# Optimization experiments

Measured on AMD Instinct MI355X. Metric: run time of the kernel, lower is better.

Reference implementation:

```python
import jax, jax.numpy as jnp
import numpy as np

NEG_SLOPE = 0.2
EPS = 1e-16

N_NODES = 50000
N_EDGES = 800000
IN_C = 256
HID_C = 64
HEADS = 4
OUT_C = 128
N_GRAPHS = 100


def setup_inputs() -> dict:
    key = jax.random.key(0)
    ks = jax.random.split(key, 12)
    x = jax.random.normal(ks[0], (N_NODES, IN_C), dtype=jnp.float32)
    edge_index = jax.random.randint(ks[1], (2, N_EDGES), 0, N_NODES, dtype=jnp.int64)
    batch = jnp.sort(jax.random.randint(ks[2], (N_NODES,), 0, N_GRAPHS, dtype=jnp.int64))
    s1 = 1.0 / np.sqrt(IN_C)
    s2 = 1.0 / np.sqrt(HEADS * HID_C)
    W1 = jax.random.uniform(ks[3], (IN_C, HEADS * HID_C), jnp.float32, -s1, s1)
    att_src1 = jax.random.uniform(ks[4], (HEADS, HID_C), jnp.float32, -s1, s1)
    att_dst1 = jax.random.uniform(ks[5], (HEADS, HID_C), jnp.float32, -s1, s1)
    bias1 = jnp.zeros((HEADS * HID_C,), jnp.float32)
    W2 = jax.random.uniform(ks[6], (HEADS * HID_C, OUT_C), jnp.float32, -s2, s2)
    att_src2 = jax.random.uniform(ks[7], (1, OUT_C), jnp.float32, -s2, s2)
    att_dst2 = jax.random.uniform(ks[8], (1, OUT_C), jnp.float32, -s2, s2)
    bias2 = jnp.zeros((OUT_C,), jnp.float32)
    return {"x": x, "W1": W1, "att_src1": att_src1, "att_dst1": att_dst1,
            "bias1": bias1, "W2": W2, "att_src2": att_src2, "att_dst2": att_dst2,
            "bias2": bias2, "edge_index": edge_index, "batch": batch,
            "num_graphs": N_GRAPHS}


def gat_conv(x, W, att_src, att_dst, bias, src, dst, heads, ch):
    # x: [N, F_in]; W: [F_in, heads*ch]; att_*: [heads, ch]
    n = x.shape[0]
    h = (x @ W).reshape(n, heads, ch)                      # [N, H, C]
    a_src = jnp.sum(h * att_src[None], axis=-1)            # [N, H]
    a_dst = jnp.sum(h * att_dst[None], axis=-1)            # [N, H]
    alpha = a_src[src] + a_dst[dst]                        # [E, H]
    alpha = jax.nn.leaky_relu(alpha, NEG_SLOPE)
    # segment softmax over destination nodes (every node has a self-loop)
    amax = jax.ops.segment_max(alpha, dst, num_segments=n)
    e = jnp.exp(alpha - amax[dst])
    denom = jax.ops.segment_sum(e, dst, num_segments=n)
    alpha = e / (denom[dst] + EPS)                         # [E, H]
    msg = h[src] * alpha[:, :, None]                       # [E, H, C]
    out = jax.ops.segment_sum(msg, dst, num_segments=n)    # [N, H, C]
    return out.reshape(n, heads * ch) + bias


def reference(x, W1, att_src1, att_dst1, bias1, W2, att_src2, att_dst2, bias2,
              edge_index, batch, num_graphs):
    n = x.shape[0]
    loops = jnp.arange(n, dtype=edge_index.dtype)
    src = jnp.concatenate([edge_index[0], loops])
    dst = jnp.concatenate([edge_index[1], loops])
    h = gat_conv(x, W1, att_src1, att_dst1, bias1, src, dst, HEADS, HID_C)
    h = jax.nn.relu(h)
    h = gat_conv(h, W2, att_src2, att_dst2, bias2, src, dst, 1, OUT_C)
    h = jax.nn.relu(h)
    # global mean pool over graphs
    sums = jax.ops.segment_sum(h, batch, num_segments=num_graphs)
    cnt = jax.ops.segment_sum(jnp.ones((n, 1), h.dtype), batch, num_segments=num_graphs)
    return sums / jnp.maximum(cnt, 1.0)
```

## Files before the change

kernel.cpp:

```cpp
#include <hip/hip_runtime.h>
#include <hip/hip_bf16.h>
#include <hip/hip_fp16.h>

#define N_NODES 50000
#define N_EDGES 800000
#define E_TOT   (N_EDGES + N_NODES)
#define IN_C    256
#define H1C     256
#define HEADS   4
#define HID_C   64
#define OUT_C   128
#define N_GRAPHS 100
#define NEG_SLOPE 0.2f
#define EPS_F 1e-16f

#define NBUCKET 391
#define SORT_BLOCKS 104
#define EDGES_PER_SB 8192
#define BH_STRIDE 392
#define STAGE_CAP 3072

#define PREP_BHIST_BLOCKS  104
#define PREP_CAST_BLOCKS   12500
#define PREP_W1_BLOCKS     256
#define PREP_W2_BLOCKS     128
#define PREP_BOUNDS_BLOCKS 196
#define PREP_DOUT_BLOCKS   50
#define PREP_TOTAL (PREP_BHIST_BLOCKS + PREP_CAST_BLOCKS + PREP_W1_BLOCKS + PREP_W2_BLOCKS + PREP_BOUNDS_BLOCKS + PREP_DOUT_BLOCKS)

typedef _Float16 half8_t __attribute__((ext_vector_type(8)));
typedef float f32x4 __attribute__((ext_vector_type(4)));

__global__ __launch_bounds__(256) void prep_kernel(const float* __restrict__ x,
                                                   _Float16* __restrict__ xh,
                                                   const float* __restrict__ W1,
                                                   _Float16* __restrict__ W1t,
                                                   const float* __restrict__ W2,
                                                   _Float16* __restrict__ W2t,
                                                   const int* __restrict__ ei,
                                                   int* __restrict__ bhist,
                                                   const int* __restrict__ batch,
                                                   int* __restrict__ gstart,
                                                   float* __restrict__ d_out) {
    __shared__ int bh[NBUCKET];
    int b = blockIdx.x;
    int tid = threadIdx.x;
    if (b < PREP_BHIST_BLOCKS) {
        for (int t = tid; t < NBUCKET; t += 256) bh[t] = 0;
        __syncthreads();
        int base = b * EDGES_PER_SB;
#pragma unroll 4
        for (int k = 0; k < EDGES_PER_SB / 256; ++k) {
            int idx = base + k * 256 + tid;
            int d = -1;
            if (idx < N_EDGES) d = ei[N_EDGES + idx];
            else if (idx < E_TOT) d = idx - N_EDGES;
            if (d >= 0 && d < N_NODES) atomicAdd(&bh[d >> 7], 1);
        }
        __syncthreads();
        for (int t = tid; t < NBUCKET; t += 256)
            bhist[b * BH_STRIDE + t] = bh[t];
        return;
    }
    b -= PREP_BHIST_BLOCKS;
    if (b < PREP_CAST_BLOCKS) {
        int idx = b * 256 + tid;
        float4 v = reinterpret_cast<const float4*>(x)[idx];
        union { _Float16 h[4]; uint2 u; } p;
        p.h[0] = (_Float16)v.x; p.h[1] = (_Float16)v.y;
        p.h[2] = (_Float16)v.z; p.h[3] = (_Float16)v.w;
        reinterpret_cast<uint2*>(xh)[idx] = p.u;
        return;
    }
    b -= PREP_CAST_BLOCKS;
    if (b < PREP_W1_BLOCKS) {
        int idx = b * 256 + tid;
        int n = idx >> 8, k = idx & 255;
        W1t[idx] = (_Float16)W1[k * 256 + n];
        return;
    }
    b -= PREP_W1_BLOCKS;
    if (b < PREP_W2_BLOCKS) {
        int idx = b * 256 + tid;
        int n = idx >> 8, k = idx & 255;
        W2t[idx] = (_Float16)W2[k * 128 + n];
        return;
    }
    b -= PREP_W2_BLOCKS;
    if (b < PREP_BOUNDS_BLOCKS) {
        int idx = b * 256 + tid;
        if (idx >= N_NODES) return;
        int g = batch[idx];
        if (g < 0) g = 0; if (g >= N_GRAPHS) g = N_GRAPHS - 1;
        if (idx == 0) {
            for (int j = 0; j <= g; ++j) gstart[j] = 0;
        } else {
            int gp = batch[idx - 1];
            if (gp < 0) gp = 0; if (gp >= N_GRAPHS) gp = N_GRAPHS - 1;
            for (int j = gp + 1; j <= g; ++j) gstart[j] = idx;
        }
        if (idx == N_NODES - 1) {
            for (int j = g + 1; j <= N_GRAPHS; ++j) gstart[j] = N_NODES;
        }
        return;
    }
    b -= PREP_BOUNDS_BLOCKS;
    {
        int idx = b * 256 + tid;
        if (idx < N_GRAPHS * 128) d_out[idx] = 0.f;
    }
}

__global__ __launch_bounds__(64) void bucket_scan(int* __restrict__ bhist,
                                                  int* __restrict__ btot) {
    int j = blockIdx.x;
    int lane = threadIdx.x;
    int carry = 0;
    for (int b0 = 0; b0 < SORT_BLOCKS; b0 += 64) {
        int b = b0 + lane;
        int v = (b < SORT_BLOCKS) ? bhist[b * BH_STRIDE + j] : 0;
        int inc = v;
#pragma unroll
        for (int off = 1; off < 64; off <<= 1) {
            int u = __shfl_up(inc, off);
            if (lane >= off) inc += u;
        }
        if (b < SORT_BLOCKS) bhist[b * BH_STRIDE + j] = inc - v + carry;
        carry += __shfl(inc, 63);
    }
    if (lane == 0) btot[j] = carry;
}

__global__ __launch_bounds__(512) void bucket_base(const int* __restrict__ btot,
                                                   int* __restrict__ bbase) {
    __shared__ int lds[512];
    int t = threadIdx.x;
    int v = (t < NBUCKET) ? btot[t] : 0;
    lds[t] = v;
    __syncthreads();
#pragma unroll
    for (int off = 1; off < 512; off <<= 1) {
        int u = (t >= off) ? lds[t - off] : 0;
        __syncthreads();
        lds[t] += u;
        __syncthreads();
    }
    if (t < NBUCKET) bbase[t] = lds[t] - v;
    if (t == NBUCKET - 1) bbase[NBUCKET] = lds[t];
}

__global__ __launch_bounds__(256) void bucket_bin(const int* __restrict__ ei,
                                                  const int* __restrict__ bbase,
                                                  const int* __restrict__ bhist,
                                                  int* __restrict__ ebuf) {
    __shared__ int cur[NBUCKET];
    int tid = threadIdx.x;
    for (int t = tid; t < NBUCKET; t += 256)
        cur[t] = bbase[t] + bhist[blockIdx.x * BH_STRIDE + t];
    __syncthreads();
    int base = blockIdx.x * EDGES_PER_SB;
#pragma unroll 4
    for (int k = 0; k < EDGES_PER_SB / 256; ++k) {
        int idx = base + k * 256 + tid;
        int s = 0, d = -1;
        if (idx < N_EDGES) { s = ei[idx]; d = ei[N_EDGES + idx]; }
        else if (idx < E_TOT) { s = idx - N_EDGES; d = s; }
        if (d >= 0 && d < N_NODES) {
            int p = atomicAdd(&cur[d >> 7], 1);
            ebuf[p] = (s & 0xFFFF) | ((d & 127) << 16);
        }
    }
}

__global__ __launch_bounds__(256) void bucket_sort(const int* __restrict__ bbase,
                                                   const int* __restrict__ ebuf,
                                                   int* __restrict__ ssrc,
                                                   int* __restrict__ row_ptr) {
    __shared__ int cnt[128];
    __shared__ int sc[128];
    __shared__ int stage[STAGE_CAP];
    int j = blockIdx.x;
    int tid = threadIdx.x;
    int jn0 = j << 7;
    int nNodes = N_NODES - jn0; if (nNodes > 128) nNodes = 128;
    int lo = bbase[j];
    int hi = bbase[j + 1];
    int span = hi - lo;
    if (tid < 128) cnt[tid] = 0;
    __syncthreads();
    for (int t = lo + tid; t < hi; t += 256)
        atomicAdd(&cnt[(ebuf[t] >> 16) & 127], 1);
    __syncthreads();
    if (tid < 128) sc[tid] = cnt[tid];
    __syncthreads();
#pragma unroll
    for (int off = 1; off < 128; off <<= 1) {
        int u = (tid >= off && tid < 128) ? sc[tid - off] : 0;
        __syncthreads();
        if (tid < 128) sc[tid] += u;
        __syncthreads();
    }
    if (tid < 128) {
        int excl = sc[tid] - cnt[tid];
        if (tid < nNodes) row_ptr[jn0 + tid] = lo + excl;
        cnt[tid] = excl;
    }
    if (j == NBUCKET - 1 && tid == 0) row_ptr[N_NODES] = hi;
    __syncthreads();
    if (span <= STAGE_CAP) {
        for (int t = lo + tid; t < hi; t += 256) {
            int v = ebuf[t];
            int p = atomicAdd(&cnt[(v >> 16) & 127], 1);
            stage[p] = v & 0xFFFF;
        }
        __syncthreads();
        for (int t = tid; t < span; t += 256) ssrc[lo + t] = stage[t];
    } else {
        for (int t = lo + tid; t < hi; t += 256) {
            int v = ebuf[t];
            int p = atomicAdd(&cnt[(v >> 16) & 127], 1);
            if (p >= 0 && p < span) ssrc[lo + p] = v & 0xFFFF;
        }
    }
}

__global__ __launch_bounds__(256) void gemm_mfma_kernel(const _Float16* __restrict__ A,
                                                        const _Float16* __restrict__ Bt,
                                                        _Float16* __restrict__ C,
                                                        int mode,
                                                        const float* __restrict__ attS,
                                                        const float* __restrict__ attD,
                                                        float* __restrict__ a_src_o,
                                                        float* __restrict__ a_dst_o,
                                                        int M, int N) {
    __shared__ _Float16 As[128][56];
    __shared__ _Float16 Bs[128][56];
    __shared__ float lds_ps[128];
    __shared__ float lds_pd[128];
    const int tid = threadIdx.x;
    const int tileM = blockIdx.x * 128;
    const int tileN = blockIdx.y * 128;
    const int w = tid >> 6, lane = tid & 63;
    const int wm = (w >> 1) * 64, wn = (w & 1) * 64;
    const int quad = lane >> 4, mlane = lane & 15;
    const int srow = tid >> 2;
    const int schunk = (tid & 3) * 8;

    f32x4 zero = {0.f, 0.f, 0.f, 0.f};
    f32x4 acc[4][4];
#pragma unroll
    for (int i = 0; i < 4; ++i)
#pragma unroll
        for (int j = 0; j < 4; ++j) acc[i][j] = zero;

    const uint4* Av = reinterpret_cast<const uint4*>(A);
    const uint4* Bv = reinterpret_cast<const uint4*>(Bt);
    const int r0 = tileM + srow, r1 = r0 + 64;
    const bool ok0 = r0 < M, ok1 = r1 < M;
    const int bn0 = tileN + srow, bn1 = bn0 + 64;
    const uint4 z4 = make_uint4(0, 0, 0, 0);

    for (int k0 = 0; k0 < 256; k0 += 32) {
        const int kc = (k0 >> 3) + (tid & 3);
        uint4 a0 = ok0 ? Av[(size_t)r0 * 32 + kc] : z4;
        uint4 a1 = ok1 ? Av[(size_t)r1 * 32 + kc] : z4;
        uint4 b0 = Bv[(size_t)bn0 * 32 + kc];
        uint4 b1 = Bv[(size_t)bn1 * 32 + kc];
        __syncthreads();
        *reinterpret_cast<uint4*>(&As[srow][schunk]) = a0;
        *reinterpret_cast<uint4*>(&As[srow + 64][schunk]) = a1;
        *reinterpret_cast<uint4*>(&Bs[srow][schunk]) = b0;
        *reinterpret_cast<uint4*>(&Bs[srow + 64][schunk]) = b1;
        __syncthreads();
        half8_t af[4], bf[4];
#pragma unroll
        for (int mt = 0; mt < 4; ++mt)
            af[mt] = *reinterpret_cast<const half8_t*>(&As[wm + mt * 16 + mlane][quad * 8]);
#pragma unroll
        for (int nt = 0; nt < 4; ++nt)
            bf[nt] = *reinterpret_cast<const half8_t*>(&Bs[wn + nt * 16 + mlane][quad * 8]);
#pragma unroll
        for (int mt = 0; mt < 4; ++mt)
#pragma unroll
            for (int nt = 0; nt < 4; ++nt)
                acc[mt][nt] = __builtin_amdgcn_mfma_f32_16x16x32_f16(af[mt], bf[nt], acc[mt][nt], 0, 0, 0);
    }
#pragma unroll
    for (int mt = 0; mt < 4; ++mt) {
#pragma unroll
        for (int i = 0; i < 4; ++i) {
            int row = tileM + wm + mt * 16 + quad * 4 + i;
            if (row < M) {
                _Float16* cp = C + (size_t)row * N + tileN + wn;
#pragma unroll
                for (int nt = 0; nt < 4; ++nt)
                    cp[nt * 16 + mlane] = (_Float16)acc[mt][nt][i];
            }
        }
    }
    if (mode == 1) {
        int hd = (tileN + wn) >> 6;
        float as[4], ad[4];
#pragma unroll
        for (int nt = 0; nt < 4; ++nt) {
            as[nt] = attS[hd * 64 + nt * 16 + mlane];
            ad[nt] = attD[hd * 64 + nt * 16 + mlane];
        }
#pragma unroll
        for (int mt = 0; mt < 4; ++mt) {
#pragma unroll
            for (int i = 0; i < 4; ++i) {
                float ps = acc[mt][0][i] * as[0] + acc[mt][1][i] * as[1]
                         + acc[mt][2][i] * as[2] + acc[mt][3][i] * as[3];
                float pd = acc[mt][0][i] * ad[0] + acc[mt][1][i] * ad[1]
                         + acc[mt][2][i] * ad[2] + acc[mt][3][i] * ad[3];
#pragma unroll
                for (int off = 1; off < 16; off <<= 1) {
                    ps += __shfl_xor(ps, off);
                    pd += __shfl_xor(pd, off);
                }
                if (mlane == 0) {
                    int row = tileM + wm + mt * 16 + quad * 4 + i;
                    if (row < M) {
                        a_src_o[row * 4 + hd] = ps;
                        a_dst_o[row * 4 + hd] = pd;
                    }
                }
            }
        }
    } else if (mode == 2) {
        float as[4], ad[4];
#pragma unroll
        for (int nt = 0; nt < 4; ++nt) {
            as[nt] = attS[wn + nt * 16 + mlane];
            ad[nt] = attD[wn + nt * 16 + mlane];
        }
        float psa[4][4], pda[4][4];
#pragma unroll
        for (int mt = 0; mt < 4; ++mt) {
#pragma unroll
            for (int i = 0; i < 4; ++i) {
                float ps = acc[mt][0][i] * as[0] + acc[mt][1][i] * as[1]
                         + acc[mt][2][i] * as[2] + acc[mt][3][i] * as[3];
                float pd = acc[mt][0][i] * ad[0] + acc[mt][1][i] * ad[1]
                         + acc[mt][2][i] * ad[2] + acc[mt][3][i] * ad[3];
#pragma unroll
                for (int off = 1; off < 16; off <<= 1) {
                    ps += __shfl_xor(ps, off);
                    pd += __shfl_xor(pd, off);
                }
                psa[mt][i] = ps; pda[mt][i] = pd;
            }
        }
        __syncthreads();
        if (wn == 0 && mlane == 0) {
#pragma unroll
            for (int mt = 0; mt < 4; ++mt)
#pragma unroll
                for (int i = 0; i < 4; ++i) {
                    int lr = wm + mt * 16 + quad * 4 + i;
                    lds_ps[lr] = psa[mt][i];
                    lds_pd[lr] = pda[mt][i];
                }
        }
        __syncthreads();
        if (wn == 64 && mlane == 0) {
#pragma unroll
            for (int mt = 0; mt < 4; ++mt)
#pragma unroll
                for (int i = 0; i < 4; ++i) {
                    int lr = wm + mt * 16 + quad * 4 + i;
                    int row = tileM + lr;
                    if (row < M) {
                        a_src_o[row] = psa[mt][i] + lds_ps[lr];
                        a_dst_o[row] = pda[mt][i] + lds_pd[lr];
                    }
                }
        }
    }
}

__device__ __forceinline__ float lrelu(float x) { return x > 0.f ? x : NEG_SLOPE * x; }

__global__ __launch_bounds__(256) void edge1_kernel(const int* __restrict__ row_ptr,
                                                    const int* __restrict__ ssrc,
                                                    const __half* __restrict__ h1h,
                                                    const float* __restrict__ a_src,
                                                    const float* __restrict__ a_dst,
                                                    const float* __restrict__ bias,
                                                    __half* __restrict__ out) {
    int node = blockIdx.x * 4 + (threadIdx.x >> 6);
    int lane = threadIdx.x & 63;
    int hf   = lane >> 5;
    int cl   = lane & 31;
    int hd   = cl >> 3;
    int start = row_ptr[node], end = row_ptr[node + 1];
    int em1 = end - 1;
    float adh = a_dst[node * 4 + hd];

    const uint4* h1v = reinterpret_cast<const uint4*>(h1h);
    float4 aA0 = make_float4(0.f,0.f,0.f,0.f), aA1 = make_float4(0.f,0.f,0.f,0.f);
    float4 aB0 = make_float4(0.f,0.f,0.f,0.f), aB1 = make_float4(0.f,0.f,0.f,0.f);
    float s = 0.f;
    for (int e = start; e < end; e += 4) {
        int e0 = e + hf;
        int e1 = e + 2 + hf;
        int i0 = ssrc[e0 <= em1 ? e0 : em1];
        int i1 = ssrc[e1 <= em1 ? e1 : em1];
        float r0 = a_src[i0 * 4 + hd];
        float r1 = a_src[i1 * 4 + hd];
        uint4 q0 = h1v[(size_t)i0 * 32 + cl];
        uint4 q1 = h1v[(size_t)i1 * 32 + cl];
        float w0 = (e0 < end) ? __expf(lrelu(r0 + adh)) : 0.f;
        float w1 = (e1 < end) ? __expf(lrelu(r1 + adh)) : 0.f;
        s += w0 + w1;
        float2 f;
        f = __half22float2(*reinterpret_cast<const __half2*>(&q0.x)); aA0.x += w0*f.x; aA0.y += w0*f.y;
        f = __half22float2(*reinterpret_cast<const __half2*>(&q0.y)); aA0.z += w0*f.x; aA0.w += w0*f.y;
        f = __half22float2(*reinterpret_cast<const __half2*>(&q0.z)); aA1.x += w0*f.x; aA1.y += w0*f.y;
        f = __half22float2(*reinterpret_cast<const __half2*>(&q0.w)); aA1.z += w0*f.x; aA1.w += w0*f.y;
        f = __half22float2(*reinterpret_cast<const __half2*>(&q1.x)); aB0.x += w1*f.x; aB0.y += w1*f.y;
        f = __half22float2(*reinterpret_cast<const __half2*>(&q1.y)); aB0.z += w1*f.x; aB0.w += w1*f.y;
        f = __half22float2(*reinterpret_cast<const __half2*>(&q1.z)); aB1.x += w1*f.x; aB1.y += w1*f.y;
        f = __half22float2(*reinterpret_cast<const __half2*>(&q1.w)); aB1.z += w1*f.x; aB1.w += w1*f.y;
    }
    float4 c0, c1;
    c0.x = aA0.x + aB0.x; c0.y = aA0.y + aB0.y; c0.z = aA0.z + aB0.z; c0.w = aA0.w + aB0.w;
    c1.x = aA1.x + aB1.x; c1.y = aA1.y + aB1.y; c1.z = aA1.z + aB1.z; c1.w = aA1.w + aB1.w;
    c0.x += __shfl_xor(c0.x, 32); c0.y += __shfl_xor(c0.y, 32);
    c0.z += __shfl_xor(c0.z, 32); c0.w += __shfl_xor(c0.w, 32);
    c1.x += __shfl_xor(c1.x, 32); c1.y += __shfl_xor(c1.y, 32);
    c1.z += __shfl_xor(c1.z, 32); c1.w += __shfl_xor(c1.w, 32);
    s += __shfl_xor(s, 32);
    float inv = 1.0f / (s + EPS_F);
    if (lane < 32) {
        const float4* b4 = reinterpret_cast<const float4*>(bias);
        float4 b0 = b4[cl * 2], b1 = b4[cl * 2 + 1];
        union { _Float16 h[8]; uint4 u; } st;
        st.h[0] = (_Float16)fmaxf(c0.x * inv + b0.x, 0.f);
        st.h[1] = (_Float16)fmaxf(c0.y * inv + b0.y, 0.f);
        st.h[2] = (_Float16)fmaxf(c0.z * inv + b0.z, 0.f);
        st.h[3] = (_Float16)fmaxf(c0.w * inv + b0.w, 0.f);
        st.h[4] = (_Float16)fmaxf(c1.x * inv + b1.x, 0.f);
        st.h[5] = (_Float16)fmaxf(c1.y * inv + b1.y, 0.f);
        st.h[6] = (_Float16)fmaxf(c1.z * inv + b1.z, 0.f);
        st.h[7] = (_Float16)fmaxf(c1.w * inv + b1.w, 0.f);
        reinterpret_cast<uint4*>(out)[(size_t)node * 32 + cl] = st.u;
    }
}

__global__ __launch_bounds__(256) void edge2_kernel(const int* __restrict__ row_ptr,
                                                    const int* __restrict__ ssrc,
                                                    const __half* __restrict__ h2h,
                                                    const float* __restrict__ a_src,
                                                    const float* __restrict__ a_dst,
                                                    const float* __restrict__ bias,
                                                    float* __restrict__ out) {
    int lane = threadIdx.x & 63;
    int node = blockIdx.x * 8 + ((threadIdx.x >> 6) << 1) + (lane >> 5);
    int sub  = (lane >> 4) & 1;
    int cl   = lane & 15;
    int start = row_ptr[node], end = row_ptr[node + 1];
    int em1 = end - 1;
    float ad = a_dst[node];

    const uint4* h2v = reinterpret_cast<const uint4*>(h2h);
    float4 aA0 = make_float4(0.f,0.f,0.f,0.f), aA1 = make_float4(0.f,0.f,0.f,0.f);
    float4 aB0 = make_float4(0.f,0.f,0.f,0.f), aB1 = make_float4(0.f,0.f,0.f,0.f);
    float s = 0.f;
    for (int e = start; e < end; e += 4) {
        int e0 = e + sub;
        int e1 = e + 2 + sub;
        int i0 = ssrc[e0 <= em1 ? e0 : em1];
        int i1 = ssrc[e1 <= em1 ? e1 : em1];
        float r0 = a_src[i0];
        float r1 = a_src[i1];
        uint4 q0 = h2v[(size_t)i0 * 16 + cl];
        uint4 q1 = h2v[(size_t)i1 * 16 + cl];
        float w0 = (e0 < end) ? __expf(lrelu(r0 + ad)) : 0.f;
        float w1 = (e1 < end) ? __expf(lrelu(r1 + ad)) : 0.f;
        s += w0 + w1;
        float2 f;
        f = __half22float2(*reinterpret_cast<const __half2*>(&q0.x)); aA0.x += w0*f.x; aA0.y += w0*f.y;
        f = __half22float2(*reinterpret_cast<const __half2*>(&q0.y)); aA0.z += w0*f.x; aA0.w += w0*f.y;
        f = __half22float2(*reinterpret_cast<const __half2*>(&q0.z)); aA1.x += w0*f.x; aA1.y += w0*f.y;
        f = __half22float2(*reinterpret_cast<const __half2*>(&q0.w)); aA1.z += w0*f.x; aA1.w += w0*f.y;
        f = __half22float2(*reinterpret_cast<const __half2*>(&q1.x)); aB0.x += w1*f.x; aB0.y += w1*f.y;
        f = __half22float2(*reinterpret_cast<const __half2*>(&q1.y)); aB0.z += w1*f.x; aB0.w += w1*f.y;
        f = __half22float2(*reinterpret_cast<const __half2*>(&q1.z)); aB1.x += w1*f.x; aB1.y += w1*f.y;
        f = __half22float2(*reinterpret_cast<const __half2*>(&q1.w)); aB1.z += w1*f.x; aB1.w += w1*f.y;
    }
    float4 c0, c1;
    c0.x = aA0.x + aB0.x; c0.y = aA0.y + aB0.y; c0.z = aA0.z + aB0.z; c0.w = aA0.w + aB0.w;
    c1.x = aA1.x + aB1.x; c1.y = aA1.y + aB1.y; c1.z = aA1.z + aB1.z; c1.w = aA1.w + aB1.w;
    c0.x += __shfl_xor(c0.x, 16); c0.y += __shfl_xor(c0.y, 16);
    c0.z += __shfl_xor(c0.z, 16); c0.w += __shfl_xor(c0.w, 16);
    c1.x += __shfl_xor(c1.x, 16); c1.y += __shfl_xor(c1.y, 16);
    c1.z += __shfl_xor(c1.z, 16); c1.w += __shfl_xor(c1.w, 16);
    s += __shfl_xor(s, 16);
    float inv = 1.0f / (s + EPS_F);
    if (sub == 0) {
        const float4* b4 = reinterpret_cast<const float4*>(bias);
        float4 b0 = b4[cl * 2], b1 = b4[cl * 2 + 1];
        float4 o0, o1;
        o0.x = fmaxf(c0.x * inv + b0.x, 0.f);
        o0.y = fmaxf(c0.y * inv + b0.y, 0.f);
        o0.z = fmaxf(c0.z * inv + b0.z, 0.f);
        o0.w = fmaxf(c0.w * inv + b0.w, 0.f);
        o1.x = fmaxf(c1.x * inv + b1.x, 0.f);
        o1.y = fmaxf(c1.y * inv + b1.y, 0.f);
        o1.z = fmaxf(c1.z * inv + b1.z, 0.f);
        o1.w = fmaxf(c1.w * inv + b1.w, 0.f);
        float4* o4 = reinterpret_cast<float4*>(out) + (size_t)node * 32 + cl * 2;
        o4[0] = o0;
        o4[1] = o1;
    }
}

#define POOL_CHUNK 64
__global__ __launch_bounds__(128) void pool_kernel(const float* __restrict__ out2,
                                                   const int* __restrict__ batch,
                                                   const int* __restrict__ gstart,
                                                   float* __restrict__ d_out) {
    int c = threadIdx.x;
    int node0 = blockIdx.x * POOL_CHUNK;
    int nodeEnd = node0 + POOL_CHUNK; if (nodeEnd > N_NODES) nodeEnd = N_NODES;
    if (node0 >= N_NODES) return;
    int gprev = batch[node0];
    float acc = 0.f;
    for (int node = node0; node < nodeEnd; ++node) {
        int g = batch[node];
        if (g != gprev) {
            if (gprev >= 0 && gprev < N_GRAPHS) {
                float cnt = (float)(gstart[gprev + 1] - gstart[gprev]);
                if (cnt < 1.f) cnt = 1.f;
                atomicAdd(&d_out[gprev * 128 + c], acc / cnt);
            }
            acc = 0.f;
            gprev = g;
        }
        acc += out2[(size_t)node * 128 + c];
    }
    if (gprev >= 0 && gprev < N_GRAPHS) {
        float cnt = (float)(gstart[gprev + 1] - gstart[gprev]);
        if (cnt < 1.f) cnt = 1.f;
        atomicAdd(&d_out[gprev * 128 + c], acc / cnt);
    }
}

extern "C" void kernel_launch(void* const* d_in, const int* in_sizes, int n_in,
                              void* d_out_v, int out_size, void* d_ws, size_t ws_size,
                              hipStream_t stream) {
    const float* x      = (const float*)d_in[0];
    const float* W1     = (const float*)d_in[1];
    const float* att_s1 = (const float*)d_in[2];
    const float* att_d1 = (const float*)d_in[3];
    const float* bias1  = (const float*)d_in[4];
    const float* W2     = (const float*)d_in[5];
    const float* att_s2 = (const float*)d_in[6];
    const float* att_d2 = (const float*)d_in[7];
    const float* bias2  = (const float*)d_in[8];
    const int*   ei     = (const int*)d_in[9];
    const int*   batch  = (const int*)d_in[10];
    float* d_out = (float*)d_out_v;

    float* ws = (float*)d_ws;
    _Float16* xh    = (_Float16*)ws;
    _Float16* h1h   = (_Float16*)(ws + 6400000);
    _Float16* out1h = (_Float16*)(ws + 12800000);
    _Float16* h2h   = (_Float16*)ws;
    float*    out2  = ws + 6400000;
    float* a_src1 = ws + 19200000;
    float* a_dst1 = a_src1 + 200000;
    float* a_src2 = a_dst1 + 200000;
    float* a_dst2 = a_src2 + 50000;
    int* row_ptr  = (int*)(a_dst2 + 50000);
    int* ssrc     = row_ptr + 50016;
    int* ebuf     = ssrc + 850000;
    int* bhist    = ebuf + 851968;
    int* btot     = bhist + (SORT_BLOCKS * BH_STRIDE);
    int* bbase    = btot + 512;
    int* gstart   = bbase + 512;
    _Float16* W1t = (_Float16*)(gstart + 128);
    _Float16* W2t = W1t + 65536;

    prep_kernel<<<PREP_TOTAL, 256, 0, stream>>>(x, xh, W1, W1t, W2, W2t,
                                                ei, bhist, batch, gstart, d_out);

    bucket_scan<<<NBUCKET, 64, 0, stream>>>(bhist, btot);
    bucket_base<<<1, 512, 0, stream>>>(btot, bbase);
    bucket_bin<<<SORT_BLOCKS, 256, 0, stream>>>(ei, bbase, bhist, ebuf);
    bucket_sort<<<NBUCKET, 256, 0, stream>>>(bbase, ebuf, ssrc, row_ptr);

    {
        dim3 g((N_NODES + 127) / 128, H1C / 128);
        gemm_mfma_kernel<<<g, 256, 0, stream>>>(xh, W1t, h1h, 1,
                                                att_s1, att_d1, a_src1, a_dst1,
                                                N_NODES, H1C);
    }
    edge1_kernel<<<N_NODES / 4, 256, 0, stream>>>(row_ptr, ssrc, (const __half*)h1h,
                                                  a_src1, a_dst1, bias1, (__half*)out1h);

    {
        dim3 g((N_NODES + 127) / 128, OUT_C / 128);
        gemm_mfma_kernel<<<g, 256, 0, stream>>>(out1h, W2t, h2h, 2,
                                                att_s2, att_d2, a_src2, a_dst2,
                                                N_NODES, OUT_C);
    }
    edge2_kernel<<<N_NODES / 8, 256, 0, stream>>>(row_ptr, ssrc, (const __half*)h2h,
                                                  a_src2, a_dst2, bias2, out2);

    pool_kernel<<<(N_NODES + POOL_CHUNK - 1) / POOL_CHUNK, 128, 0, stream>>>(out2, batch, gstart, d_out);
}
```

Measured before the change: 302.2 us.

## Replace multi-pass bucket sort with atomic bucket offsets and fuse sort with GEMM1

Result: no change. 299.6 us (-0.9%).

```diff
diff --git a/kernel.cpp b/kernel.cpp
--- a/kernel.cpp
+++ b/kernel.cpp
@@ -15,18 +15,18 @@
 #define EPS_F 1e-16f
 
 #define NBUCKET 391
-#define SORT_BLOCKS 104
+#define BIN_BLOCKS 104
 #define EDGES_PER_SB 8192
-#define BH_STRIDE 392
-#define STAGE_CAP 3072
-
-#define PREP_BHIST_BLOCKS  104
+#define EBUF_CAP 4096
+#define STAGE_CAP 4096
+#define GEMM1_MB 391
+
 #define PREP_CAST_BLOCKS   12500
 #define PREP_W1_BLOCKS     256
 #define PREP_W2_BLOCKS     128
 #define PREP_BOUNDS_BLOCKS 196
-#define PREP_DOUT_BLOCKS   50
-#define PREP_TOTAL (PREP_BHIST_BLOCKS + PREP_CAST_BLOCKS + PREP_W1_BLOCKS + PREP_W2_BLOCKS + PREP_BOUNDS_BLOCKS + PREP_DOUT_BLOCKS)
+#define PREP_ZERO_BLOCKS   52
+#define PREP_TOTAL (PREP_CAST_BLOCKS + PREP_W1_BLOCKS + PREP_W2_BLOCKS + PREP_BOUNDS_BLOCKS + PREP_ZERO_BLOCKS)
 
 typedef _Float16 half8_t __attribute__((ext_vector_type(8)));
 typedef float f32x4 __attribute__((ext_vector_type(4)));
@@ -37,32 +37,12 @@
                                                    _Float16* __restrict__ W1t,
                                                    const float* __restrict__ W2,
                                                    _Float16* __restrict__ W2t,
-                                                   const int* __restrict__ ei,
-                                                   int* __restrict__ bhist,
                                                    const int* __restrict__ batch,
                                                    int* __restrict__ gstart,
+                                                   int* __restrict__ gcur,
                                                    float* __restrict__ d_out) {
-    __shared__ int bh[NBUCKET];
     int b = blockIdx.x;
     int tid = threadIdx.x;
-    if (b < PREP_BHIST_BLOCKS) {
-        for (int t = tid; t < NBUCKET; t += 256) bh[t] = 0;
-        __syncthreads();
-        int base = b * EDGES_PER_SB;
-#pragma unroll 4
-        for (int k = 0; k < EDGES_PER_SB / 256; ++k) {
-            int idx = base + k * 256 + tid;
-            int d = -1;
-            if (idx < N_EDGES) d = ei[N_EDGES + idx];
-            else if (idx < E_TOT) d = idx - N_EDGES;
-            if (d >= 0 && d < N_NODES) atomicAdd(&bh[d >> 7], 1);
-        }
-        __syncthreads();
-        for (int t = tid; t < NBUCKET; t += 256)
-            bhist[b * BH_STRIDE + t] = bh[t];
-        return;
-    }
-    b -= PREP_BHIST_BLOCKS;
     if (b < PREP_CAST_BLOCKS) {
         int idx = b * 256 + tid;
         float4 v = reinterpret_cast<const float4*>(x)[idx];
@@ -108,57 +88,37 @@
     {
         int idx = b * 256 + tid;
         if (idx < N_GRAPHS * 128) d_out[idx] = 0.f;
-    }
-}
-
-__global__ __launch_bounds__(64) void bucket_scan(int* __restrict__ bhist,
-                                                  int* __restrict__ btot) {
-    int j = blockIdx.x;
-    int lane = threadIdx.x;
-    int carry = 0;
-    for (int b0 = 0; b0 < SORT_BLOCKS; b0 += 64) {
-        int b = b0 + lane;
-        int v = (b < SORT_BLOCKS) ? bhist[b * BH_STRIDE + j] : 0;
-        int inc = v;
-#pragma unroll
-        for (int off = 1; off < 64; off <<= 1) {
-            int u = __shfl_up(inc, off);
-            if (lane >= off) inc += u;
-        }
-        if (b < SORT_BLOCKS) bhist[b * BH_STRIDE + j] = inc - v + carry;
-        carry += __shfl(inc, 63);
-    }
-    if (lane == 0) btot[j] = carry;
-}
-
-__global__ __launch_bounds__(512) void bucket_base(const int* __restrict__ btot,
-                                                   int* __restrict__ bbase) {
-    __shared__ int lds[512];
-    int t = threadIdx.x;
-    int v = (t < NBUCKET) ? btot[t] : 0;
-    lds[t] = v;
-    __syncthreads();
-#pragma unroll
-    for (int off = 1; off < 512; off <<= 1) {
-        int u = (t >= off) ? lds[t - off] : 0;
-        __syncthreads();
-        lds[t] += u;
-        __syncthreads();
-    }
-    if (t < NBUCKET) bbase[t] = lds[t] - v;
-    if (t == NBUCKET - 1) bbase[NBUCKET] = lds[t];
+        else {
+            int k = idx - N_GRAPHS * 128;
+            if (k < 512) gcur[k] = 0;
+        }
+    }
 }
 
 __global__ __launch_bounds__(256) void bucket_bin(const int* __restrict__ ei,
-                                                  const int* __restrict__ bbase,
-                                                  const int* __restrict__ bhist,
+                                                  int* __restrict__ gcur,
                                                   int* __restrict__ ebuf) {
-    __shared__ int cur[NBUCKET];
+    __shared__ int bh[NBUCKET];
+    __shared__ int bofs[NBUCKET];
     int tid = threadIdx.x;
-    for (int t = tid; t < NBUCKET; t += 256)
-        cur[t] = bbase[t] + bhist[blockIdx.x * BH_STRIDE + t];
+    for (int t = tid; t < NBUCKET; t += 256) bh[t] = 0;
     __syncthreads();
     int base = blockIdx.x * EDGES_PER_SB;
+#pragma unroll 4
+    for (int k = 0; k < EDGES_PER_SB / 256; ++k) {
+        int idx = base + k * 256 + tid;
+        int d = -1;
+        if (idx < N_EDGES) d = ei[N_EDGES + idx];
+        else if (idx < E_TOT) d = idx - N_EDGES;
+        if (d >= 0 && d < N_NODES) atomicAdd(&bh[d >> 7], 1);
+    }
+    __syncthreads();
+    for (int t = tid; t < NBUCKET; t += 256) {
+        int c = bh[t];
+        bofs[t] = (c > 0) ? atomicAdd(&gcur[t], c) : 0;
+        bh[t] = 0;
+    }
+    __syncthreads();
 #pragma unroll 4
     for (int k = 0; k < EDGES_PER_SB / 256; ++k) {
         int idx = base + k * 256 + tid;
@@ -166,60 +126,175 @@
         if (idx < N_EDGES) { s = ei[idx]; d = ei[N_EDGES + idx]; }
         else if (idx < E_TOT) { s = idx - N_EDGES; d = s; }
         if (d >= 0 && d < N_NODES) {
-            int p = atomicAdd(&cur[d >> 7], 1);
-            ebuf[p] = (s & 0xFFFF) | ((d & 127) << 16);
-        }
-    }
-}
-
-__global__ __launch_bounds__(256) void bucket_sort(const int* __restrict__ bbase,
-                                                   const int* __restrict__ ebuf,
-                                                   int* __restrict__ ssrc,
-                                                   int* __restrict__ row_ptr) {
-    __shared__ int cnt[128];
-    __shared__ int sc[128];
-    __shared__ int stage[STAGE_CAP];
-    int j = blockIdx.x;
-    int tid = threadIdx.x;
-    int jn0 = j << 7;
-    int nNodes = N_NODES - jn0; if (nNodes > 128) nNodes = 128;
-    int lo = bbase[j];
-    int hi = bbase[j + 1];
-    int span = hi - lo;
-    if (tid < 128) cnt[tid] = 0;
-    __syncthreads();
-    for (int t = lo + tid; t < hi; t += 256)
-        atomicAdd(&cnt[(ebuf[t] >> 16) & 127], 1);
-    __syncthreads();
-    if (tid < 128) sc[tid] = cnt[tid];
-    __syncthreads();
-#pragma unroll
-    for (int off = 1; off < 128; off <<= 1) {
-        int u = (tid >= off && tid < 128) ? sc[tid - off] : 0;
-        __syncthreads();
-        if (tid < 128) sc[tid] += u;
-        __syncthreads();
-    }
-    if (tid < 128) {
-        int excl = sc[tid] - cnt[tid];
-        if (tid < nNodes) row_ptr[jn0 + tid] = lo + excl;
-        cnt[tid] = excl;
-    }
-    if (j == NBUCKET - 1 && tid == 0) row_ptr[N_NODES] = hi;
-    __syncthreads();
-    if (span <= STAGE_CAP) {
-        for (int t = lo + tid; t < hi; t += 256) {
-            int v = ebuf[t];
+            int t = d >> 7;
+            int p = bofs[t] + atomicAdd(&bh[t], 1);
+            if (p < EBUF_CAP)
+                ebuf[t * EBUF_CAP + p] = (s & 0xFFFF) | ((d & 127) << 16);
+        }
+    }
+}
+
+__global__ __launch_bounds__(256) void sort_gemm1_kernel(const int* __restrict__ gcur,
+                                                         const int* __restrict__ ebuf,
+                                                         int* __restrict__ ssrc,
+                                                         int* __restrict__ row_ptr,
+                                                         const _Float16* __restrict__ A,
+                                                         const _Float16* __restrict__ Bt,
+                                                         _Float16* __restrict__ C,
+                                                         const float* __restrict__ attS,
+                                                         const float* __restrict__ attD,
+                                                         float* __restrict__ a_src_o,
+                                                         float* __restrict__ a_dst_o) {
+    __shared__ __align__(16) char smem[29696];
+    __shared__ int s_off;
+    const int tid = threadIdx.x;
+
+    if (blockIdx.x < NBUCKET) {
+        int* cnt   = reinterpret_cast<int*>(smem);
+        int* sc    = cnt + 128;
+        int* stage = sc + 128;
+        int j = blockIdx.x;
+        if (tid < 64) {
+            int acc = 0;
+            for (int i = tid; i < j; i += 64) {
+                int c = gcur[i];
+                acc += (c < EBUF_CAP) ? c : EBUF_CAP;
+            }
+#pragma unroll
+            for (int off = 32; off > 0; off >>= 1) acc += __shfl_down(acc, off);
+            if (tid == 0) s_off = acc;
+        }
+        if (tid < 128) cnt[tid] = 0;
+        __syncthreads();
+        int span = gcur[j]; if (span > EBUF_CAP) span = EBUF_CAP;
+        int lo = s_off;
+        const int* eb = ebuf + j * EBUF_CAP;
+        for (int t = tid; t < span; t += 256)
+            atomicAdd(&cnt[(eb[t] >> 16) & 127], 1);
+        __syncthreads();
+        if (tid < 128) sc[tid] = cnt[tid];
+        __syncthreads();
+#pragma unroll
+        for (int off = 1; off < 128; off <<= 1) {
+            int u = (tid >= off && tid < 128) ? sc[tid - off] : 0;
+            __syncthreads();
+            if (tid < 128) sc[tid] += u;
+            __syncthreads();
+        }
+        int jn0 = j << 7;
+        int nNodes = N_NODES - jn0; if (nNodes > 128) nNodes = 128;
+        if (tid < 128) {
+            int excl = sc[tid] - cnt[tid];
+            if (tid < nNodes) row_ptr[jn0 + tid] = lo + excl;
+            cnt[tid] = excl;
+        }
+        if (j == NBUCKET - 1 && tid == 0) row_ptr[N_NODES] = lo + span;
+        __syncthreads();
+        for (int t = tid; t < span; t += 256) {
+            int v = eb[t];
             int p = atomicAdd(&cnt[(v >> 16) & 127], 1);
             stage[p] = v & 0xFFFF;
         }
         __syncthreads();
         for (int t = tid; t < span; t += 256) ssrc[lo + t] = stage[t];
-    } else {
-        for (int t = lo + tid; t < hi; t += 256) {
-            int v = ebuf[t];
-            int p = atomicAdd(&cnt[(v >> 16) & 127], 1);
-            if (p >= 0 && p < span) ssrc[lo + p] = v & 0xFFFF;
+        return;
+    }
+
+    _Float16 (*As)[56] = reinterpret_cast<_Float16(*)[56]>(smem);
+    _Float16 (*Bs)[56] = reinterpret_cast<_Float16(*)[56]>(smem + 14336);
+    float* lds_ps = reinterpret_cast<float*>(smem + 28672);
+    float* lds_pd = reinterpret_cast<float*>(smem + 29184);
+    (void)lds_ps; (void)lds_pd;
+    int b2 = blockIdx.x - NBUCKET;
+    const int tileM = (b2 >= GEMM1_MB ? b2 - GEMM1_MB : b2) * 128;
+    const int tileN = (b2 >= GEMM1_MB) ? 128 : 0;
+    const int w = tid >> 6, lane = tid & 63;
+    const int wm = (w >> 1) * 64, wn = (w & 1) * 64;
+    const int quad = lane >> 4, mlane = lane & 15;
+    const int srow = tid >> 2;
+    const int schunk = (tid & 3) * 8;
+
+    f32x4 zero = {0.f, 0.f, 0.f, 0.f};
+    f32x4 acc[4][4];
+#pragma unroll
+    for (int i = 0; i < 4; ++i)
+#pragma unroll
+        for (int j = 0; j < 4; ++j) acc[i][j] = zero;
+
+    const uint4* Av = reinterpret_cast<const uint4*>(A);
+    const uint4* Bv = reinterpret_cast<const uint4*>(Bt);
+    const int r0 = tileM + srow, r1 = r0 + 64;
+    const bool ok0 = r0 < N_NODES, ok1 = r1 < N_NODES;
+    const int bn0 = tileN + srow, bn1 = bn0 + 64;
+    const uint4 z4 = make_uint4(0, 0, 0, 0);
+
+    for (int k0 = 0; k0 < 256; k0 += 32) {
+        const int kc = (k0 >> 3) + (tid & 3);
+        uint4 a0 = ok0 ? Av[(size_t)r0 * 32 + kc] : z4;
+        uint4 a1 = ok1 ? Av[(size_t)r1 * 32 + kc] : z4;
+        uint4 b0 = Bv[(size_t)bn0 * 32 + kc];
+        uint4 b1 = Bv[(size_t)bn1 * 32 + kc];
+        __syncthreads();
+        *reinterpret_cast<uint4*>(&As[srow][schunk]) = a0;
+        *reinterpret_cast<uint4*>(&As[srow + 64][schunk]) = a1;
+        *reinterpret_cast<uint4*>(&Bs[srow][schunk]) = b0;
+        *reinterpret_cast<uint4*>(&Bs[srow + 64][schunk]) = b1;
+        __syncthreads();
+        half8_t af[4], bf[4];
+#pragma unroll
+        for (int mt = 0; mt < 4; ++mt)
+            af[mt] = *reinterpret_cast<const half8_t*>(&As[wm + mt * 16 + mlane][quad * 8]);
+#pragma unroll
+        for (int nt = 0; nt < 4; ++nt)
+            bf[nt] = *reinterpret_cast<const half8_t*>(&Bs[wn + nt * 16 + mlane][quad * 8]);
+#pragma unroll
+        for (int mt = 0; mt < 4; ++mt)
+#pragma unroll
+            for (int nt = 0; nt < 4; ++nt)
+                acc[mt][nt] = __builtin_amdgcn_mfma_f32_16x16x32_f16(af[mt], bf[nt], acc[mt][nt], 0, 0, 0);
+    }
+#pragma unroll
+    for (int mt = 0; mt < 4; ++mt) {
+#pragma unroll
+        for (int i = 0; i < 4; ++i) {
+            int row = tileM + wm + mt * 16 + quad * 4 + i;
+            if (row < N_NODES) {
+                _Float16* cp = C + (size_t)row * 256 + tileN + wn;
+#pragma unroll
+                for (int nt = 0; nt < 4; ++nt)
+                    cp[nt * 16 + mlane] = (_Float16)acc[mt][nt][i];
+            }
+        }
+    }
+    {
+        int hd = (tileN + wn) >> 6;
+        float as[4], ad[4];
+#pragma unroll
+        for (int nt = 0; nt < 4; ++nt) {
+            as[nt] = attS[hd * 64 + nt * 16 + mlane];
+            ad[nt] = attD[hd * 64 + nt * 16 + mlane];
+        }
+#pragma unroll
+        for (int mt = 0; mt < 4; ++mt) {
+#pragma unroll
+            for (int i = 0; i < 4; ++i) {
+                float ps = acc[mt][0][i] * as[0] + acc[mt][1][i] * as[1]
+                         + acc[mt][2][i] * as[2] + acc[mt][3][i] * as[3];
+                float pd = acc[mt][0][i] * ad[0] + acc[mt][1][i] * ad[1]
+                         + acc[mt][2][i] * ad[2] + acc[mt][3][i] * ad[3];
+#pragma unroll
+                for (int off = 1; off < 16; off <<= 1) {
+                    ps += __shfl_xor(ps, off);
+                    pd += __shfl_xor(pd, off);
+                }
+                if (mlane == 0) {
+                    int row = tileM + wm + mt * 16 + quad * 4 + i;
+                    if (row < N_NODES) {
+                        a_src_o[row * 4 + hd] = ps;
+                        a_dst_o[row * 4 + hd] = pd;
+                    }
+                }
+            }
         }
     }
 }
@@ -227,7 +302,6 @@
 __global__ __launch_bounds__(256) void gemm_mfma_kernel(const _Float16* __restrict__ A,
                                                         const _Float16* __restrict__ Bt,
                                                         _Float16* __restrict__ C,
-                                                        int mode,
                                                         const float* __restrict__ attS,
                                                         const float* __restrict__ attD,
                                                         float* __restrict__ a_src_o,
@@ -239,7 +313,7 @@
     __shared__ float lds_pd[128];
     const int tid = threadIdx.x;
     const int tileM = blockIdx.x * 128;
-    const int tileN = blockIdx.y * 128;
+    const int tileN = 0;
     const int w = tid >> 6, lane = tid & 63;
     const int wm = (w >> 1) * 64, wn = (w & 1) * 64;
     const int quad = lane >> 4, mlane = lane & 15;
@@ -298,37 +372,7 @@
             }
         }
     }
-    if (mode == 1) {
-        int hd = (tileN + wn) >> 6;
-        float as[4], ad[4];
-#pragma unroll
-        for (int nt = 0; nt < 4; ++nt) {
-            as[nt] = attS[hd * 64 + nt * 16 + mlane];
-            ad[nt] = attD[hd * 64 + nt * 16 + mlane];
-        }
-#pragma unroll
-        for (int mt = 0; mt < 4; ++mt) {
-#pragma unroll
-            for (int i = 0; i < 4; ++i) {
-                float ps = acc[mt][0][i] * as[0] + acc[mt][1][i] * as[1]
-                         + acc[mt][2][i] * as[2] + acc[mt][3][i] * as[3];
-                float pd = acc[mt][0][i] * ad[0] + acc[mt][1][i] * ad[1]
-                         + acc[mt][2][i] * ad[2] + acc[mt][3][i] * ad[3];
-#pragma unroll
-                for (int off = 1; off < 16; off <<= 1) {
-                    ps += __shfl_xor(ps, off);
-                    pd += __shfl_xor(pd, off);
-                }
-                if (mlane == 0) {
-                    int row = tileM + wm + mt * 16 + quad * 4 + i;
-                    if (row < M) {
-                        a_src_o[row * 4 + hd] = ps;
-                        a_dst_o[row * 4 + hd] = pd;
-                    }
-                }
-            }
-        }
-    } else if (mode == 2) {
+    {
         float as[4], ad[4];
 #pragma unroll
         for (int nt = 0; nt < 4; ++nt) {
@@ -577,36 +621,26 @@
     int* row_ptr  = (int*)(a_dst2 + 50000);
     int* ssrc     = row_ptr + 50016;
     int* ebuf     = ssrc + 850000;
-    int* bhist    = ebuf + 851968;
-    int* btot     = bhist + (SORT_BLOCKS * BH_STRIDE);
-    int* bbase    = btot + 512;
-    int* gstart   = bbase + 512;
+    int* gcur     = ebuf + (NBUCKET * EBUF_CAP);
+    int* gstart   = gcur + 512;
     _Float16* W1t = (_Float16*)(gstart + 128);
     _Float16* W2t = W1t + 65536;
 
     prep_kernel<<<PREP_TOTAL, 256, 0, stream>>>(x, xh, W1, W1t, W2, W2t,
-                                                ei, bhist, batch, gstart, d_out);
-
-    bucket_scan<<<NBUCKET, 64, 0, stream>>>(bhist, btot);
-    bucket_base<<<1, 512, 0, stream>>>(btot, bbase);
-    bucket_bin<<<SORT_BLOCKS, 256, 0, stream>>>(ei, bbase, bhist, ebuf);
-    bucket_sort<<<NBUCKET, 256, 0, stream>>>(bbase, ebuf, ssrc, row_ptr);
-
-    {
-        dim3 g((N_NODES + 127) / 128, H1C / 128);
-        gemm_mfma_kernel<<<g, 256, 0, stream>>>(xh, W1t, h1h, 1,
-                                                att_s1, att_d1, a_src1, a_dst1,
-                                                N_NODES, H1C);
-    }
+                                                batch, gstart, gcur, d_out);
+
+    bucket_bin<<<BIN_BLOCKS, 256, 0, stream>>>(ei, gcur, ebuf);
+
+    sort_gemm1_kernel<<<NBUCKET + GEMM1_MB * 2, 256, 0, stream>>>(
+        gcur, ebuf, ssrc, row_ptr, xh, W1t, h1h,
+        att_s1, att_d1, a_src1, a_dst1);
+
     edge1_kernel<<<N_NODES / 4, 256, 0, stream>>>(row_ptr, ssrc, (const __half*)h1h,
                                                   a_src1, a_dst1, bias1, (__half*)out1h);
 
-    {
-        dim3 g((N_NODES + 127) / 128, OUT_C / 128);
-        gemm_mfma_kernel<<<g, 256, 0, stream>>>(out1h, W2t, h2h, 2,
-                                                att_s2, att_d2, a_src2, a_dst2,
-                                                N_NODES, OUT_C);
-    }
+    gemm_mfma_kernel<<<(N_NODES + 127) / 128, 256, 0, stream>>>(
+        out1h, W2t, h2h, att_s2, att_d2, a_src2, a_dst2, N_NODES, OUT_C);
+
     edge2_kernel<<<N_NODES / 8, 256, 0, stream>>>(row_ptr, ssrc, (const __half*)h2h,
                                                   a_src2, a_dst2, bias2, out2);
 
```
